# Optimization experiments

Measured on AMD Instinct MI355X. Metric: run time of the kernel, lower is better.

## Reference

```python
import math
import jax, jax.numpy as jnp
import numpy as np

B, H, S, D = 2, 16, 2048, 64

def setup_inputs() -> dict:
    key = jax.random.key(0)
    kq, kk, kv = jax.random.split(key, 3)
    return {
        "query": jax.random.normal(kq, (B, H, S, D), dtype=jnp.float32),
        "key": jax.random.normal(kk, (B, H, S, D), dtype=jnp.float32),
        "value": jax.random.normal(kv, (B, H, S, D), dtype=jnp.float32),
        "mask": jnp.ones((B, S, 1), dtype=jnp.float32),  # padding mask, 1 = keep
        "mask_now": 0,  # 0 -> causal (tril diag=0); 1 -> strict causal (diag=-1)
    }

def reference(query, key, value, mask, mask_now):
    d_k = query.shape[-1]
    seq_len = mask.shape[1]
    # [B,H,S,S] scaled scores
    attn_scores = jnp.einsum("bhqd,bhkd->bhqk", query, key) / math.sqrt(d_k)
    diag = -1 if mask_now else 0
    triu_mask = jnp.tril(jnp.ones((seq_len, seq_len), dtype=mask.dtype), diag)  # [S,S]
    # mask[:, :, 0] -> per-query padding mask broadcast over key dim: [B,1,S,S]
    full_mask = triu_mask[None, None, :, :] * mask[:, None, :, 0:1]
    attn_scores = jnp.where(full_mask == 0, jnp.float32(-1e9), attn_scores)
    attn_scores = jax.nn.softmax(attn_scores, axis=-1)
    output = jnp.einsum("bhqk,bhkd->bhqd", attn_scores, value)
    return (output, attn_scores)
```

## Files before the change

kernel.cpp:

```cpp
#include <hip/hip_runtime.h>
#include <math.h>

#define NB 2
#define NH 16
#define SL 2048
#define DD 64
#define KC 64
#define NCH (SL / KC)
#define NT 256
#define SLW 68

typedef short bf16x8 __attribute__((ext_vector_type(8)));
typedef float f32x4  __attribute__((ext_vector_type(4)));

__device__ __forceinline__ unsigned short f2bf(float x) {
    unsigned u = __float_as_uint(x);
    u += 0x7fffu + ((u >> 16) & 1u);
    return (unsigned short)(u >> 16);
}

__device__ __forceinline__ void lds_barrier() {
    asm volatile("s_waitcnt lgkmcnt(0)\n\ts_barrier" ::: "memory");
}

__device__ __forceinline__ void gl_lds16(const void* src, void* dst) {
    __builtin_amdgcn_global_load_lds(
        (const __attribute__((address_space(1))) void*)src,
        (__attribute__((address_space(3))) void*)dst, 16, 0, 0);
}

__global__ __launch_bounds__(256)
void cvt_bf16(const float* __restrict__ in, unsigned short* __restrict__ out,
              int n4, float scale)
{
    int i = blockIdx.x * 256 + threadIdx.x;
    if (i >= n4) return;
    float4 v = ((const float4*)in)[i];
    ushort4 o;
    o.x = f2bf(v.x * scale); o.y = f2bf(v.y * scale);
    o.z = f2bf(v.z * scale); o.w = f2bf(v.w * scale);
    ((ushort4*)out)[i] = o;
}

__global__ __launch_bounds__(256)
void transpose_v(const float* __restrict__ V, unsigned short* __restrict__ Vt)
{
    __shared__ __align__(16) unsigned short vt[64 * 72];
    const int bh = blockIdx.x >> 5;
    const int s0 = (blockIdx.x & 31) * 64;
    const int t  = threadIdx.x;

    const float4* src = (const float4*)(V + ((size_t)bh * SL + s0) * DD);
    #pragma unroll
    for (int i = 0; i < 4; ++i) {
        int idx = t + i * 256;
        int r = idx >> 4, d4 = idx & 15;
        float4 v = src[r * 16 + d4];
        vt[(d4 * 4 + 0) * 72 + r] = f2bf(v.x);
        vt[(d4 * 4 + 1) * 72 + r] = f2bf(v.y);
        vt[(d4 * 4 + 2) * 72 + r] = f2bf(v.z);
        vt[(d4 * 4 + 3) * 72 + r] = f2bf(v.w);
    }
    __syncthreads();
    const int d = t >> 2, seg = t & 3;
    unsigned short* dst = Vt + ((size_t)bh * DD + d) * SL + s0 + seg * 16;
    uint4 p0 = *(const uint4*)&vt[d * 72 + seg * 16];
    uint4 p1 = *(const uint4*)&vt[d * 72 + seg * 16 + 8];
    *(uint4*)dst = p0;
    *(uint4*)(dst + 8) = p1;
}

__global__ __launch_bounds__(NT, 4)
void attn_mfma(const unsigned short* __restrict__ Qb,
               const unsigned short* __restrict__ Kb,
               const unsigned short* __restrict__ Vt,
               const float* __restrict__ Mg,
               const int* __restrict__ MNg,
               float* __restrict__ Og)
{
    __shared__ __align__(16) unsigned short kst[2][KC * DD];
    __shared__ __align__(16) unsigned short vst[DD * KC];
    __shared__ __align__(16) float slab[32 * SLW];
    __shared__ float lsx[4][16];

    const int tid  = threadIdx.x;
    const int w    = tid >> 6;
    const int lane = tid & 63;
    const int l15  = lane & 15;
    const int qd   = lane >> 4;
    const int rowhalf = w >> 1;
    const int colhalf = w & 1;

    const int lin  = blockIdx.x;
    const int xcd  = lin & 7;
    const int iloc = lin >> 3;
    const int g    = iloc & 31;
    const int bh   = xcd * 4 + (iloc >> 5);
    const int b    = bh >> 4;
    const int diag = (MNg[0] != 0) ? -1 : 0;

    const unsigned short* Qh  = Qb + (size_t)bh * SL * DD;
    const unsigned short* Kh  = Kb + (size_t)bh * SL * DD;
    const unsigned short* Vth = Vt + (size_t)bh * DD * SL;
    float* Sb = Og + (size_t)NB * NH * SL * DD + (size_t)bh * SL * SL;
    float* Ob = Og + (size_t)bh * SL * DD;

    const int srw = lane >> 3;
    const int sc16 = (lane & 7) ^ srw;

    auto stageK = [&](int kc, int dbuf) {
        const unsigned short* base = Kh + (size_t)kc * KC * DD;
        #pragma unroll
        for (int j = 0; j < 2; ++j) {
            int i = w * 2 + j;
            const unsigned short* src = base + (size_t)(i * 8 + srw) * DD + sc16 * 8;
            gl_lds16(src, &kst[dbuf][i * 512]);
        }
    };
    auto stageV = [&](int c0) {
        #pragma unroll
        for (int j = 0; j < 2; ++j) {
            int i = w * 2 + j;
            const unsigned short* src = Vth + (size_t)(i * 8 + srw) * SL + c0 + sc16 * 8;
            gl_lds16(src, &vst[i * 512]);
        }
    };
    auto rd16 = [&](const unsigned short* lb, int r, int c16) -> bf16x8 {
        int a = (r * 128 + c16 * 16) ^ ((r & 7) << 4);
        return *(const bf16x8*)((const char*)lb + a);
    };

    for (int sweep = 0; sweep < 2; ++sweep) {
        const int R0 = sweep ? (2016 - g * 32) : (g * 32);

        int degflag = 0;
        if (lane < 32) {
            int row = R0 + lane;
            float m = Mg[(size_t)b * SL + row];
            degflag = (m == 0.0f) || (row + diag < 0);
        }
        const bool deg32 = __any(degflag);
        const int N = deg32 ? NCH : (((R0 + 31 + diag) >> 6) + 1);

        int rlim[4];
        #pragma unroll
        for (int reg = 0; reg < 4; ++reg) {
            int row = R0 + rowhalf * 16 + qd * 4 + reg;
            float m = Mg[(size_t)b * SL + row];
            int rl = row + diag;
            if (m == 0.0f) rl = -1;
            rlim[reg] = rl;
        }

        const unsigned short* qrow = Qh + (size_t)(R0 + rowhalf * 16 + l15) * DD + qd * 8;
        bf16x8 qf0 = *(const bf16x8*)qrow;
        bf16x8 qf1 = *(const bf16x8*)(qrow + 32);

        float lacc[4] = {0.0f, 0.0f, 0.0f, 0.0f};
        stageK(0, 0);
        asm volatile("s_waitcnt vmcnt(0)" ::: "memory");
        lds_barrier();
        for (int kc = 0; kc < N; ++kc) {
            const int d = kc & 1;
            if (kc + 1 < N) stageK(kc + 1, d ^ 1);
            const int c0 = kc * KC;
            #pragma unroll
            for (int t = 0; t < 2; ++t) {
                const int ntg = colhalf * 2 + t;
                bf16x8 b0 = rd16(kst[d], ntg * 16 + l15, qd);
                bf16x8 b1 = rd16(kst[d], ntg * 16 + l15, 4 + qd);
                f32x4 acc = {0.0f, 0.0f, 0.0f, 0.0f};
                __builtin_amdgcn_s_setprio(1);
                acc = __builtin_amdgcn_mfma_f32_16x16x32_bf16(qf0, b0, acc, 0, 0, 0);
                acc = __builtin_amdgcn_mfma_f32_16x16x32_bf16(qf1, b1, acc, 0, 0, 0);
                __builtin_amdgcn_s_setprio(0);
                const int col = c0 + ntg * 16 + l15;
                #pragma unroll
                for (int reg = 0; reg < 4; ++reg)
                    lacc[reg] += (col <= rlim[reg]) ? __builtin_exp2f(acc[reg]) : 0.0f;
            }
            asm volatile("s_waitcnt vmcnt(0)" ::: "memory");
            lds_barrier();
        }

        float lsum[4];
        #pragma unroll
        for (int reg = 0; reg < 4; ++reg) {
            float s = lacc[reg];
            s += __shfl_xor(s, 1);  s += __shfl_xor(s, 2);
            s += __shfl_xor(s, 4);  s += __shfl_xor(s, 8);
            lsum[reg] = s;
        }
        if (l15 == 0) {
            #pragma unroll
            for (int reg = 0; reg < 4; ++reg)
                lsx[w][qd * 4 + reg] = lsum[reg];
        }
        lds_barrier();
        float pmul[4], pfill[4];
        #pragma unroll
        for (int reg = 0; reg < 4; ++reg) {
            float tot = lsum[reg] + lsx[w ^ 1][qd * 4 + reg];
            pmul[reg]  = (rlim[reg] < 0) ? 0.0f : 1.0f / tot;
            pfill[reg] = (rlim[reg] < 0) ? (1.0f / (float)SL) : 0.0f;
        }

        f32x4 oacc[2];
        oacc[0] = (f32x4){0.0f, 0.0f, 0.0f, 0.0f};
        oacc[1] = (f32x4){0.0f, 0.0f, 0.0f, 0.0f};

        stageK(0, 0);
        asm volatile("s_waitcnt vmcnt(0)" ::: "memory");
        lds_barrier();
        for (int kc = 0; kc < N; ++kc) {
            const int d  = kc & 1;
            const int c0 = kc * KC;
            stageV(c0);
            const bool pk = (kc + 1 < N);
            if (pk) stageK(kc + 1, d ^ 1);
            #pragma unroll
            for (int t = 0; t < 2; ++t) {
                const int ntg = colhalf * 2 + t;
                bf16x8 b0 = rd16(kst[d], ntg * 16 + l15, qd);
                bf16x8 b1 = rd16(kst[d], ntg * 16 + l15, 4 + qd);
                f32x4 acc = {0.0f, 0.0f, 0.0f, 0.0f};
                __builtin_amdgcn_s_setprio(1);
                acc = __builtin_amdgcn_mfma_f32_16x16x32_bf16(qf0, b0, acc, 0, 0, 0);
                acc = __builtin_amdgcn_mfma_f32_16x16x32_bf16(qf1, b1, acc, 0, 0, 0);
                __builtin_amdgcn_s_setprio(0);
                const int col = c0 + ntg * 16 + l15;
                #pragma unroll
                for (int reg = 0; reg < 4; ++reg) {
                    float val = (col <= rlim[reg]) ? __builtin_exp2f(acc[reg]) * pmul[reg]
                                                   : pfill[reg];
                    slab[(rowhalf * 16 + qd * 4 + reg) * SLW + ntg * 16 + l15] = val;
                }
            }
            if (pk) { asm volatile("s_waitcnt vmcnt(2)" ::: "memory"); }
            else    { asm volatile("s_waitcnt vmcnt(0)" ::: "memory"); }
            lds_barrier();
            #pragma unroll
            for (int ii = 0; ii < 2; ++ii) {
                int rr = w * 8 + ii * 4 + (lane >> 4);
                int c4 = lane & 15;
                *(float4*)(Sb + (size_t)(R0 + rr) * SL + c0 + c4 * 4) =
                    *(const float4*)&slab[rr * SLW + c4 * 4];
            }
            #pragma unroll
            for (int ks = 0; ks < 2; ++ks) {
                const float* pr = &slab[(rowhalf * 16 + l15) * SLW + ks * 32 + qd * 8];
                float4 x = *(const float4*)pr;
                float4 y = *(const float4*)(pr + 4);
                bf16x8 f;
                f[0] = (short)f2bf(x.x); f[1] = (short)f2bf(x.y);
                f[2] = (short)f2bf(x.z); f[3] = (short)f2bf(x.w);
                f[4] = (short)f2bf(y.x); f[5] = (short)f2bf(y.y);
                f[6] = (short)f2bf(y.z); f[7] = (short)f2bf(y.w);
                #pragma unroll
                for (int nt = 0; nt < 2; ++nt) {
                    bf16x8 v = rd16(vst, colhalf * 32 + nt * 16 + l15, ks * 4 + qd);
                    __builtin_amdgcn_s_setprio(1);
                    oacc[nt] = __builtin_amdgcn_mfma_f32_16x16x32_bf16(f, v, oacc[nt], 0, 0, 0);
                    __builtin_amdgcn_s_setprio(0);
                }
            }
            if (pk) {
                asm volatile("s_waitcnt vmcnt(2)" ::: "memory");
                lds_barrier();
            }
        }
        lds_barrier();

        {
            const int zc0 = N * KC;
            float4 z = make_float4(0.0f, 0.0f, 0.0f, 0.0f);
            for (int i = 0; i < 8; ++i) {
                float* rowp = Sb + (size_t)(R0 + w * 8 + i) * SL;
                for (int c = zc0 + (lane << 2); c < SL; c += 256)
                    *(float4*)(rowp + c) = z;
            }
        }

        #pragma unroll
        for (int nt = 0; nt < 2; ++nt)
            #pragma unroll
            for (int reg = 0; reg < 4; ++reg)
                slab[(rowhalf * 16 + qd * 4 + reg) * SLW + colhalf * 32 + nt * 16 + l15] =
                    oacc[nt][reg];
        lds_barrier();
        #pragma unroll
        for (int ii = 0; ii < 2; ++ii) {
            int rr = w * 8 + ii * 4 + (lane >> 4);
            int c4 = lane & 15;
            *(float4*)(Ob + (size_t)(R0 + rr) * DD + c4 * 4) =
                *(const float4*)&slab[rr * SLW + c4 * 4];
        }
        lds_barrier();
    }
}

extern "C" void kernel_launch(void* const* d_in, const int* in_sizes, int n_in,
                              void* d_out, int out_size, void* d_ws, size_t ws_size,
                              hipStream_t stream)
{
    const float* q  = (const float*)d_in[0];
    const float* k  = (const float*)d_in[1];
    const float* v  = (const float*)d_in[2];
    const float* mk = (const float*)d_in[3];
    const int*   mn = (const int*)d_in[4];
    float* out = (float*)d_out;

    const size_t nElem = (size_t)NB * NH * SL * DD;
    unsigned short* Qb = (unsigned short*)d_ws;
    unsigned short* Kp = Qb + nElem;
    unsigned short* Vp = Kp + nElem;

    const int n4 = (int)(nElem / 4);
    cvt_bf16<<<n4 / 256, 256, 0, stream>>>(q, Qb, n4, 0.125f * 1.44269504f);
    cvt_bf16<<<n4 / 256, 256, 0, stream>>>(k, Kp, n4, 1.0f);
    transpose_v<<<NB * NH * (SL / 64), 256, 0, stream>>>(v, Vp);

    attn_mfma<<<1024, NT, 0, stream>>>(Qb, Kp, Vp, mk, mn, out);
}
```

Measured before the change: 648.8 us.

## Triple-buffer K in the row-sum pass and relax vmcnt waits in the output pass

The first pass (softmax denominators) moves from double-buffered K with a full vmcnt(0) wait plus barrier per chunk to a three-slot ring. The next chunk's prefetch can now stay in flight (vmcnt(2)) with only one barrier per iteration. The V staging buffer is folded into the third slot so LDS use does not grow. In the second pass the end-of-iteration wait drops to vmcnt(8), so outstanding score-matrix global stores no longer stall the loop. An extra barrier guards the lsx exchange. The risk is subtle LDS reuse hazards across the ring slots and the aliased V buffer.

```diff
diff --git a/kernel.cpp b/kernel.cpp
--- a/kernel.cpp
+++ b/kernel.cpp
@@ -22,6 +22,7 @@
 __device__ __forceinline__ void lds_barrier() {
     asm volatile("s_waitcnt lgkmcnt(0)\n\ts_barrier" ::: "memory");
 }
+#define WAITV(n) asm volatile("s_waitcnt vmcnt(" #n ")" ::: "memory")
 
 __device__ __forceinline__ void gl_lds16(const void* src, void* dst) {
     __builtin_amdgcn_global_load_lds(
@@ -78,8 +79,7 @@
                const int* __restrict__ MNg,
                float* __restrict__ Og)
 {
-    __shared__ __align__(16) unsigned short kst[2][KC * DD];
-    __shared__ __align__(16) unsigned short vst[DD * KC];
+    __shared__ __align__(16) unsigned short kb[3][KC * DD];
     __shared__ __align__(16) float slab[32 * SLW];
     __shared__ float lsx[4][16];
 
@@ -114,7 +114,7 @@
         for (int j = 0; j < 2; ++j) {
             int i = w * 2 + j;
             const unsigned short* src = base + (size_t)(i * 8 + srw) * DD + sc16 * 8;
-            gl_lds16(src, &kst[dbuf][i * 512]);
+            gl_lds16(src, &kb[dbuf][i * 512]);
         }
     };
     auto stageV = [&](int c0) {
@@ -122,7 +122,7 @@
         for (int j = 0; j < 2; ++j) {
             int i = w * 2 + j;
             const unsigned short* src = Vth + (size_t)(i * 8 + srw) * SL + c0 + sc16 * 8;
-            gl_lds16(src, &vst[i * 512]);
+            gl_lds16(src, &kb[2][i * 512]);
         }
     };
     auto rd16 = [&](const unsigned short* lb, int r, int c16) -> bf16x8 {
@@ -158,17 +158,17 @@
 
         float lacc[4] = {0.0f, 0.0f, 0.0f, 0.0f};
         stageK(0, 0);
-        asm volatile("s_waitcnt vmcnt(0)" ::: "memory");
-        lds_barrier();
         for (int kc = 0; kc < N; ++kc) {
-            const int d = kc & 1;
-            if (kc + 1 < N) stageK(kc + 1, d ^ 1);
+            const int d = kc % 3;
+            if (kc + 1 < N) { stageK(kc + 1, (kc + 1) % 3); WAITV(2); }
+            else            { WAITV(0); }
+            lds_barrier();
             const int c0 = kc * KC;
             #pragma unroll
             for (int t = 0; t < 2; ++t) {
                 const int ntg = colhalf * 2 + t;
-                bf16x8 b0 = rd16(kst[d], ntg * 16 + l15, qd);
-                bf16x8 b1 = rd16(kst[d], ntg * 16 + l15, 4 + qd);
+                bf16x8 b0 = rd16(kb[d], ntg * 16 + l15, qd);
+                bf16x8 b1 = rd16(kb[d], ntg * 16 + l15, 4 + qd);
                 f32x4 acc = {0.0f, 0.0f, 0.0f, 0.0f};
                 __builtin_amdgcn_s_setprio(1);
                 acc = __builtin_amdgcn_mfma_f32_16x16x32_bf16(qf0, b0, acc, 0, 0, 0);
@@ -179,8 +179,6 @@
                 for (int reg = 0; reg < 4; ++reg)
                     lacc[reg] += (col <= rlim[reg]) ? __builtin_exp2f(acc[reg]) : 0.0f;
             }
-            asm volatile("s_waitcnt vmcnt(0)" ::: "memory");
-            lds_barrier();
         }
 
         float lsum[4];
@@ -191,6 +189,7 @@
             s += __shfl_xor(s, 4);  s += __shfl_xor(s, 8);
             lsum[reg] = s;
         }
+        lds_barrier();
         if (l15 == 0) {
             #pragma unroll
             for (int reg = 0; reg < 4; ++reg)
@@ -210,19 +209,19 @@
         oacc[1] = (f32x4){0.0f, 0.0f, 0.0f, 0.0f};
 
         stageK(0, 0);
-        asm volatile("s_waitcnt vmcnt(0)" ::: "memory");
+        WAITV(0);
         lds_barrier();
         for (int kc = 0; kc < N; ++kc) {
             const int d  = kc & 1;
             const int c0 = kc * KC;
+            const bool pk = (kc + 1 < N);
             stageV(c0);
-            const bool pk = (kc + 1 < N);
             if (pk) stageK(kc + 1, d ^ 1);
             #pragma unroll
             for (int t = 0; t < 2; ++t) {
                 const int ntg = colhalf * 2 + t;
-                bf16x8 b0 = rd16(kst[d], ntg * 16 + l15, qd);
-                bf16x8 b1 = rd16(kst[d], ntg * 16 + l15, 4 + qd);
+                bf16x8 b0 = rd16(kb[d], ntg * 16 + l15, qd);
+                bf16x8 b1 = rd16(kb[d], ntg * 16 + l15, 4 + qd);
                 f32x4 acc = {0.0f, 0.0f, 0.0f, 0.0f};
                 __builtin_amdgcn_s_setprio(1);
                 acc = __builtin_amdgcn_mfma_f32_16x16x32_bf16(qf0, b0, acc, 0, 0, 0);
@@ -236,8 +235,7 @@
                     slab[(rowhalf * 16 + qd * 4 + reg) * SLW + ntg * 16 + l15] = val;
                 }
             }
-            if (pk) { asm volatile("s_waitcnt vmcnt(2)" ::: "memory"); }
-            else    { asm volatile("s_waitcnt vmcnt(0)" ::: "memory"); }
+            if (pk) { WAITV(2); } else { WAITV(0); }
             lds_barrier();
             #pragma unroll
             for (int ii = 0; ii < 2; ++ii) {
@@ -258,18 +256,15 @@
                 f[6] = (short)f2bf(y.z); f[7] = (short)f2bf(y.w);
                 #pragma unroll
                 for (int nt = 0; nt < 2; ++nt) {
-                    bf16x8 v = rd16(vst, colhalf * 32 + nt * 16 + l15, ks * 4 + qd);
+                    bf16x8 v = rd16(kb[2], colhalf * 32 + nt * 16 + l15, ks * 4 + qd);
                     __builtin_amdgcn_s_setprio(1);
                     oacc[nt] = __builtin_amdgcn_mfma_f32_16x16x32_bf16(f, v, oacc[nt], 0, 0, 0);
                     __builtin_amdgcn_s_setprio(0);
                 }
             }
-            if (pk) {
-                asm volatile("s_waitcnt vmcnt(2)" ::: "memory");
-                lds_barrier();
-            }
-        }
-        lds_barrier();
+            if (pk) { WAITV(8); }
+            lds_barrier();
+        }
 
         {
             const int zc0 = N * KC;
```

Result: no change. 648.2 us (-0.1%).
